# Optimization experiments

Measured on AMD Instinct MI355X. Metric: run time of the kernel, lower is better.

## Reference

```python
import jax, jax.numpy as jnp
import numpy as np

D_MODEL = 512
D_K = 64
D_V = 64
N_HEADS = 8
N = 4096
EPS = 1e-5


def setup_inputs() -> dict:
    key = jax.random.key(0)
    ks = jax.random.split(key, 12)
    s = 1.0 / np.sqrt(D_MODEL)
    return {
        "Q": jax.random.normal(ks[0], (N, D_MODEL), dtype=jnp.float32),
        "K": jax.random.normal(ks[1], (N, D_MODEL), dtype=jnp.float32),
        "V": jax.random.normal(ks[2], (N, D_MODEL), dtype=jnp.float32),
        "W_Q": jax.random.normal(ks[3], (D_K * N_HEADS, D_MODEL), dtype=jnp.float32) * s,
        "b_Q": jnp.zeros((D_K * N_HEADS,), jnp.float32),
        "W_K": jax.random.normal(ks[4], (D_K * N_HEADS, D_MODEL), dtype=jnp.float32) * s,
        "b_K": jnp.zeros((D_K * N_HEADS,), jnp.float32),
        "W_V": jax.random.normal(ks[5], (D_V * N_HEADS, D_MODEL), dtype=jnp.float32) * s,
        "b_V": jnp.zeros((D_V * N_HEADS,), jnp.float32),
        "W_O": jax.random.normal(ks[6], (D_MODEL, N_HEADS * D_V), dtype=jnp.float32) * s,
        "b_O": jnp.zeros((D_MODEL,), jnp.float32),
        "gamma": jnp.ones((D_MODEL,), jnp.float32),
        "beta": jnp.zeros((D_MODEL,), jnp.float32),
    }


def reference(Q, K, V, W_Q, b_Q, W_K, b_K, W_V, b_V, W_O, b_O, gamma, beta):
    n = Q.shape[0]
    # projections (torch Linear: x @ W.T + b), then split heads: [N, H, dk]
    Qs = (Q @ W_Q.T + b_Q).reshape(n, N_HEADS, D_K)
    Ks = (K @ W_K.T + b_K).reshape(n, N_HEADS, D_K)
    Vs = (V @ W_V.T + b_V).reshape(n, N_HEADS, D_V)
    # per-head scaled dot-product attention over the N dim, batched via einsum
    scores = jnp.einsum("nhd,mhd->hnm", Qs, Ks) / np.sqrt(D_K)  # [H, N, N]
    attn = jax.nn.softmax(scores, axis=-1)
    ctx = jnp.einsum("hnm,mhd->nhd", attn, Vs)  # [N, H, dv]
    context = ctx.reshape(n, N_HEADS * D_V)  # concat heads (matches torch.cat order)
    out = context @ W_O.T + b_O + Q  # output proj + residual
    # LayerNorm over last dim
    mu = jnp.mean(out, axis=-1, keepdims=True)
    var = jnp.mean((out - mu) ** 2, axis=-1, keepdims=True)
    return (out - mu) * jax.lax.rsqrt(var + EPS) * gamma + beta
```

## Files before the change

kernel.cpp:

```cpp
#include <hip/hip_runtime.h>
#include <cstdint>

#define N_TOK 4096
#define DMODEL 512
#define NHEADS 8
#define HDIM 64

typedef unsigned short u16;
typedef __bf16 bf16x8 __attribute__((ext_vector_type(8)));
typedef float f32x4 __attribute__((ext_vector_type(4)));

union U128 { uint4 u; bf16x8 b; u16 s[8]; };

__device__ __forceinline__ u16 f2bf(float f) {
  uint32_t u = __builtin_bit_cast(uint32_t, f);
  u += 0x7FFFu + ((u >> 16) & 1u);
  return (u16)(u >> 16);
}
__device__ __forceinline__ float bf2f(u16 s) {
  uint32_t u = ((uint32_t)s) << 16;
  return __builtin_bit_cast(float, u);
}

#if __has_builtin(__builtin_amdgcn_exp2f)
#define EXP2(x) __builtin_amdgcn_exp2f(x)
#else
#define EXP2(x) __expf((x) * 0.6931471805599453f)
#endif

__device__ __forceinline__ uint32_t cvtpk(float lo, float hi) {
  uint32_t r;
  asm("v_cvt_pk_bf16_f32 %0, %1, %2" : "=v"(r) : "v"(lo), "v"(hi));
  return r;
}

__device__ __forceinline__ void ldg2lds16(const void* g, void* s) {
  __builtin_amdgcn_global_load_lds(
      (const __attribute__((address_space(1))) void*)g,
      (__attribute__((address_space(3))) void*)s, 16, 0, 0);
}

__global__ __launch_bounds__(256) void cvt7_kernel(
    const float* __restrict__ Q, const float* __restrict__ K, const float* __restrict__ V,
    const float* __restrict__ WQ, const float* __restrict__ WK, const float* __restrict__ WV,
    const float* __restrict__ WO,
    u16* __restrict__ Qb, u16* __restrict__ Kb, u16* __restrict__ Vb,
    u16* __restrict__ WQb, u16* __restrict__ WKb, u16* __restrict__ WVb,
    u16* __restrict__ WOb)
{
  int b = blockIdx.x;
  const float* src; u16* dst; int rel;
  if      (b < 2048) { src = Q;  dst = Qb;  rel = b; }
  else if (b < 4096) { src = K;  dst = Kb;  rel = b - 2048; }
  else if (b < 6144) { src = V;  dst = Vb;  rel = b - 4096; }
  else if (b < 6400) { src = WQ; dst = WQb; rel = b - 6144; }
  else if (b < 6656) { src = WK; dst = WKb; rel = b - 6400; }
  else if (b < 6912) { src = WV; dst = WVb; rel = b - 6656; }
  else               { src = WO; dst = WOb; rel = b - 6912; }
  int i = (rel * 256 + threadIdx.x) * 4;
  float4 f = *(const float4*)(src + i);
  ushort4 o;
  o.x = f2bf(f.x); o.y = f2bf(f.y); o.z = f2bf(f.z); o.w = f2bf(f.w);
  *(ushort4*)(dst + i) = o;
}

__global__ __launch_bounds__(256) void proj3_kernel(
    const u16* __restrict__ Qb, const u16* __restrict__ Kb, const u16* __restrict__ Vb,
    const u16* __restrict__ WQb, const u16* __restrict__ WKb, const u16* __restrict__ WVb,
    const float* __restrict__ bQ, const float* __restrict__ bK, const float* __restrict__ bV,
    u16* __restrict__ Qs, u16* __restrict__ Ks, u16* __restrict__ Vt)
{
  const int z = blockIdx.z;
  const u16* A      = (z == 0) ? Qb : (z == 1) ? Kb : Vb;
  const u16* W      = (z == 0) ? WQb : (z == 1) ? WKb : WVb;
  const float* bias = (z == 0) ? bQ : (z == 1) ? bK : bV;

  const int m0 = blockIdx.x * 128;
  const int j0 = blockIdx.y * 64;
  const int tid = threadIdx.x;
  const int w = tid >> 6, lane = tid & 63, quad = lane >> 4, l = lane & 15;

  __shared__ bf16x8 sA[2][8][128];
  __shared__ bf16x8 sB[2][8][64];

  const f32x4 zero = {0.f, 0.f, 0.f, 0.f};
  f32x4 acc[2][4];
#pragma unroll
  for (int m = 0; m < 2; ++m)
#pragma unroll
    for (int s = 0; s < 4; ++s) acc[m][s] = zero;

  auto stage = [&](int kt, int buf) {
    const int k0 = kt * 64;
#pragma unroll
    for (int i = 0; i < 4; ++i) {
      const int chunk = 2 * w + (i >> 1), half = (i & 1) * 64;
      const u16* ag = A + (size_t)(m0 + half + lane) * DMODEL + k0 + chunk * 8;
      ldg2lds16(ag, (char*)&sA[buf][chunk][half]);
    }
#pragma unroll
    for (int i = 0; i < 2; ++i) {
      const int chunk = 2 * w + i;
      const u16* bg = W + (size_t)(j0 + lane) * DMODEL + k0 + chunk * 8;
      ldg2lds16(bg, (char*)&sB[buf][chunk][0]);
    }
  };

  stage(0, 0);
  __syncthreads();
  for (int kt = 0; kt < 8; ++kt) {
    const int buf = kt & 1;
    if (kt + 1 < 8) stage(kt + 1, buf ^ 1);
#pragma unroll
    for (int c = 0; c < 2; ++c) {
      bf16x8 af0 = sA[buf][c * 4 + quad][w * 32 + l];
      bf16x8 af1 = sA[buf][c * 4 + quad][w * 32 + 16 + l];
#pragma unroll
      for (int s = 0; s < 4; ++s) {
        bf16x8 bfb = sB[buf][c * 4 + quad][s * 16 + l];
        acc[0][s] = __builtin_amdgcn_mfma_f32_16x16x32_bf16(af0, bfb, acc[0][s], 0, 0, 0);
        acc[1][s] = __builtin_amdgcn_mfma_f32_16x16x32_bf16(af1, bfb, acc[1][s], 0, 0, 0);
      }
    }
    __syncthreads();
  }

#pragma unroll
  for (int m = 0; m < 2; ++m)
#pragma unroll
    for (int s = 0; s < 4; ++s) {
      int j = j0 + s * 16 + l;
      float bv = bias[j];
      int n0 = m0 + w * 32 + m * 16 + quad * 4;
      if (z < 2) {
        u16* Y = (z == 0) ? Qs : Ks;
#pragma unroll
        for (int r = 0; r < 4; ++r)
          Y[(size_t)(n0 + r) * DMODEL + j] = f2bf(acc[m][s][r] + bv);
      } else {
        ushort4 pk;
        pk.x = f2bf(acc[m][s][0] + bv); pk.y = f2bf(acc[m][s][1] + bv);
        pk.z = f2bf(acc[m][s][2] + bv); pk.w = f2bf(acc[m][s][3] + bv);
        *(ushort4*)(Vt + (size_t)j * N_TOK + n0) = pk;
      }
    }
}

__global__ __launch_bounds__(512, 4) void attn_kernel(
    const u16* __restrict__ Qs, const u16* __restrict__ Ks,
    const u16* __restrict__ Vt, u16* __restrict__ Opart, float* __restrict__ Lpart)
{
  const int hs = blockIdx.x;
  const int h = hs & 7, split = hs >> 3;
  const int qt = blockIdx.y;
  const int tid = threadIdx.x;
  const int w = tid >> 6, lane = tid & 63, quad = lane >> 4, l = lane & 15;

  __shared__ bf16x8 kch[2][8][64];
  __shared__ bf16x8 vch[2][8][64];
  __shared__ __align__(128) u16 pbuf[8][32][64];

  const int wq0 = qt * 256 + w * 32;

  bf16x8 qf[2][2];
#pragma unroll
  for (int c = 0; c < 2; ++c)
#pragma unroll
    for (int m = 0; m < 2; ++m) {
      U128 u;
      u.u = *(const uint4*)(Qs + (size_t)(wq0 + m * 16 + l) * DMODEL + h * HDIM + c * 32 + quad * 8);
#pragma unroll
      for (int j = 0; j < 8; ++j) u.s[j] = f2bf(bf2f(u.s[j]) * 0.18033688f);
      qf[c][m] = u.b;
    }

  U128 onesu;
#pragma unroll
  for (int j = 0; j < 8; ++j) onesu.s[j] = 0x3F80;

  const f32x4 zero = {0.f, 0.f, 0.f, 0.f};
  f32x4 o[2][4];
  f32x4 ol[2];
  ol[0] = zero; ol[1] = zero;
#pragma unroll
  for (int m = 0; m < 2; ++m)
#pragma unroll
    for (int s = 0; s < 4; ++s) o[m][s] = zero;

  auto stage = [&](int it, int buf) {
    const int j0 = split * 1024 + it * 64;
    if (w < 4) {
      const u16* kg = Ks + (size_t)(j0 + lane) * DMODEL + h * HDIM + w * 16;
      ldg2lds16(kg,     (char*)&kch[buf][2 * w][0]);
      ldg2lds16(kg + 8, (char*)&kch[buf][2 * w + 1][0]);
    } else {
      const int w2 = w - 4;
      const u16* vg = Vt + (size_t)(h * HDIM + lane) * N_TOK + j0 + w2 * 16;
      ldg2lds16(vg,     (char*)&vch[buf][2 * w2][0]);
      ldg2lds16(vg + 8, (char*)&vch[buf][2 * w2 + 1][0]);
    }
  };

  stage(0, 0);
  __syncthreads();

  const unsigned swz = (unsigned)((l & 7) << 4);

  for (int it = 0; it < 16; ++it) {
    const int buf = it & 1;
    if (it + 1 < 16) stage(it + 1, buf ^ 1);

#pragma unroll
    for (int kh = 0; kh < 2; ++kh) {
#pragma unroll
      for (int tt = 0; tt < 2; ++tt) {
        const int t = kh * 2 + tt;
        f32x4 sacc[2];
        sacc[0] = zero; sacc[1] = zero;
#pragma unroll
        for (int c = 0; c < 2; ++c) {
          bf16x8 kf = kch[buf][c * 4 + quad][t * 16 + l];
          sacc[0] = __builtin_amdgcn_mfma_f32_16x16x32_bf16(kf, qf[c][0], sacc[0], 0, 0, 0);
          sacc[1] = __builtin_amdgcn_mfma_f32_16x16x32_bf16(kf, qf[c][1], sacc[1], 0, 0, 0);
        }
#pragma unroll
        for (int m = 0; m < 2; ++m) {
          uint2 st;
          st.x = cvtpk(EXP2(sacc[m][0]), EXP2(sacc[m][1]));
          st.y = cvtpk(EXP2(sacc[m][2]), EXP2(sacc[m][3]));
          char* pb = (char*)&pbuf[w][m * 16 + l][0];
          *(uint2*)(pb + (((unsigned)(tt * 32 + quad * 8)) ^ swz)) = st;
        }
      }
      U128 pf0, pf1;
      const unsigned ro = ((unsigned)(quad * 16)) ^ swz;
      pf0.u = *(const uint4*)((const char*)&pbuf[w][l][0] + ro);
      pf1.u = *(const uint4*)((const char*)&pbuf[w][16 + l][0] + ro);
#pragma unroll
      for (int s = 0; s < 4; ++s) {
        bf16x8 vf = vch[buf][kh * 4 + quad][s * 16 + l];
        o[0][s] = __builtin_amdgcn_mfma_f32_16x16x32_bf16(pf0.b, vf, o[0][s], 0, 0, 0);
        o[1][s] = __builtin_amdgcn_mfma_f32_16x16x32_bf16(pf1.b, vf, o[1][s], 0, 0, 0);
      }
      ol[0] = __builtin_amdgcn_mfma_f32_16x16x32_bf16(pf0.b, onesu.b, ol[0], 0, 0, 0);
      ol[1] = __builtin_amdgcn_mfma_f32_16x16x32_bf16(pf1.b, onesu.b, ol[1], 0, 0, 0);
    }
    __syncthreads();
  }

  if (l == 0) {
    float* Lp = Lpart + ((size_t)split * NHEADS + h) * N_TOK + wq0;
#pragma unroll
    for (int m = 0; m < 2; ++m)
#pragma unroll
      for (int r = 0; r < 4; ++r)
        Lp[m * 16 + quad * 4 + r] = ol[m][r];
  }
  u16* Ob = Opart + ((size_t)(split * NHEADS + h) * N_TOK + wq0) * 64;
#pragma unroll
  for (int m = 0; m < 2; ++m)
#pragma unroll
    for (int s = 0; s < 4; ++s)
#pragma unroll
      for (int r = 0; r < 4; ++r)
        Ob[(size_t)(m * 16 + quad * 4 + r) * 64 + s * 16 + l] = f2bf(o[m][s][r]);
}

__global__ __launch_bounds__(256) void combine_kernel(
    const u16* __restrict__ Opart, const float* __restrict__ Lpart,
    u16* __restrict__ ctx)
{
  int idx = blockIdx.x * 256 + threadIdx.x;
  int n = idx >> 6;
  int c8 = idx & 63;
  int h = c8 >> 3;
  int vd0 = (c8 & 7) * 8;

  float acc[8] = {0, 0, 0, 0, 0, 0, 0, 0};
  float lsum = 0.f;
#pragma unroll
  for (int s = 0; s < 4; ++s) {
    U128 u;
    u.u = *(const uint4*)(Opart + ((size_t)(s * NHEADS + h) * N_TOK + n) * 64 + vd0);
#pragma unroll
    for (int j = 0; j < 8; ++j) acc[j] += bf2f(u.s[j]);
    lsum += Lpart[((size_t)s * NHEADS + h) * N_TOK + n];
  }
  float inv = 1.f / lsum;
  U128 u;
#pragma unroll
  for (int j = 0; j < 8; ++j) u.s[j] = f2bf(acc[j] * inv);
  *(uint4*)(ctx + (size_t)n * DMODEL + h * HDIM + vd0) = u.u;
}

__global__ __launch_bounds__(256) void gemmo_kernel(
    const u16* __restrict__ ctx, const u16* __restrict__ WOb,
    const float* __restrict__ bO, const float* __restrict__ resid,
    float* __restrict__ Y)
{
  const int m0 = blockIdx.x * 64;
  const int j0 = blockIdx.y * 64;
  const int tid = threadIdx.x;
  const int w = tid >> 6, lane = tid & 63, quad = lane >> 4, l = lane & 15;

  __shared__ bf16x8 sA[2][8][64];
  __shared__ bf16x8 sB[2][8][64];

  const f32x4 zero = {0.f, 0.f, 0.f, 0.f};
  f32x4 acc[4];
#pragma unroll
  for (int s = 0; s < 4; ++s) acc[s] = zero;

  auto stage = [&](int kt, int buf) {
    const int k0 = kt * 64;
#pragma unroll
    for (int i = 0; i < 2; ++i) {
      const int chunk = 2 * w + i;
      const u16* ag = ctx + (size_t)(m0 + lane) * DMODEL + k0 + chunk * 8;
      ldg2lds16(ag, (char*)&sA[buf][chunk][0]);
      const u16* bg = WOb + (size_t)(j0 + lane) * DMODEL + k0 + chunk * 8;
      ldg2lds16(bg, (char*)&sB[buf][chunk][0]);
    }
  };

  stage(0, 0);
  __syncthreads();
  for (int kt = 0; kt < 8; ++kt) {
    const int buf = kt & 1;
    if (kt + 1 < 8) stage(kt + 1, buf ^ 1);
#pragma unroll
    for (int c = 0; c < 2; ++c) {
      bf16x8 af = sA[buf][c * 4 + quad][w * 16 + l];
#pragma unroll
      for (int s = 0; s < 4; ++s) {
        bf16x8 bfb = sB[buf][c * 4 + quad][s * 16 + l];
        acc[s] = __builtin_amdgcn_mfma_f32_16x16x32_bf16(af, bfb, acc[s], 0, 0, 0);
      }
    }
    __syncthreads();
  }
#pragma unroll
  for (int s = 0; s < 4; ++s) {
    int j = j0 + s * 16 + l;
    float bv = bO[j];
    int n0 = m0 + w * 16 + quad * 4;
#pragma unroll
    for (int r = 0; r < 4; ++r)
      Y[(size_t)(n0 + r) * DMODEL + j] = acc[s][r] + bv + resid[(size_t)(n0 + r) * DMODEL + j];
  }
}

__global__ __launch_bounds__(256) void ln_kernel(
    const float* __restrict__ X, const float* __restrict__ gamma,
    const float* __restrict__ beta, float* __restrict__ Y)
{
  const int w = threadIdx.x >> 6, lane = threadIdx.x & 63;
  const int row = blockIdx.x * 4 + w;
  const float* x = X + (size_t)row * DMODEL + lane * 8;
  float4 a = *(const float4*)x;
  float4 b = *(const float4*)(x + 4);

  float s = a.x + a.y + a.z + a.w + b.x + b.y + b.z + b.w;
#pragma unroll
  for (int m = 1; m < 64; m <<= 1) s += __shfl_xor(s, m);
  float mu = s * (1.f / DMODEL);

  float d0 = a.x - mu, d1 = a.y - mu, d2 = a.z - mu, d3 = a.w - mu;
  float d4 = b.x - mu, d5 = b.y - mu, d6 = b.z - mu, d7 = b.w - mu;
  float v = d0*d0 + d1*d1 + d2*d2 + d3*d3 + d4*d4 + d5*d5 + d6*d6 + d7*d7;
#pragma unroll
  for (int m = 1; m < 64; m <<= 1) v += __shfl_xor(v, m);
  float sc = rsqrtf(v * (1.f / DMODEL) + 1e-5f);

  const float* g = gamma + lane * 8;
  const float* be = beta + lane * 8;
  float4 go = *(const float4*)g;
  float4 g1 = *(const float4*)(g + 4);
  float4 bo = *(const float4*)be;
  float4 b1 = *(const float4*)(be + 4);

  float4 y0, y1;
  y0.x = d0 * sc * go.x + bo.x;  y0.y = d1 * sc * go.y + bo.y;
  y0.z = d2 * sc * go.z + bo.z;  y0.w = d3 * sc * go.w + bo.w;
  y1.x = d4 * sc * g1.x + b1.x;  y1.y = d5 * sc * g1.y + b1.y;
  y1.z = d6 * sc * g1.z + b1.z;  y1.w = d7 * sc * g1.w + b1.w;

  float* yp = Y + (size_t)row * DMODEL + lane * 8;
  *(float4*)yp = y0;
  *(float4*)(yp + 4) = y1;
}

extern "C" void kernel_launch(void* const* d_in, const int* in_sizes, int n_in,
                              void* d_out, int out_size, void* d_ws, size_t ws_size,
                              hipStream_t stream)
{
  const float* Q     = (const float*)d_in[0];
  const float* K     = (const float*)d_in[1];
  const float* V     = (const float*)d_in[2];
  const float* WQ    = (const float*)d_in[3];
  const float* bQ    = (const float*)d_in[4];
  const float* WK    = (const float*)d_in[5];
  const float* bK    = (const float*)d_in[6];
  const float* WV    = (const float*)d_in[7];
  const float* bV    = (const float*)d_in[8];
  const float* WO    = (const float*)d_in[9];
  const float* bO    = (const float*)d_in[10];
  const float* gamma = (const float*)d_in[11];
  const float* beta  = (const float*)d_in[12];

  const size_t MB = 1ull << 20;
  char* ws = (char*)d_ws;
  u16* Qb   = (u16*)(ws + 0 * MB);
  u16* Kb   = (u16*)(ws + 4 * MB);
  u16* Vb   = (u16*)(ws + 8 * MB);
  u16* WQb  = (u16*)(ws + 12 * MB);
  u16* WKb  = (u16*)(ws + 12 * MB + 512 * 1024);
  u16* WVb  = (u16*)(ws + 13 * MB);
  u16* WOb  = (u16*)(ws + 13 * MB + 512 * 1024);
  u16* Qs   = (u16*)(ws + 14 * MB);
  u16* Ks   = (u16*)(ws + 18 * MB);
  u16* Vt   = (u16*)(ws + 22 * MB);
  u16* ctx  = (u16*)(ws + 26 * MB);
  u16* Opart = (u16*)(ws + 30 * MB);
  float* tmp = (float*)(ws + 30 * MB);
  float* Lpart = (float*)(ws + 46 * MB);
  float* out = (float*)d_out;

  cvt7_kernel<<<7168, 256, 0, stream>>>(Q, K, V, WQ, WK, WV, WO,
                                        Qb, Kb, Vb, WQb, WKb, WVb, WOb);
  proj3_kernel<<<dim3(32, 8, 3), 256, 0, stream>>>(Qb, Kb, Vb, WQb, WKb, WVb,
                                                   bQ, bK, bV, Qs, Ks, Vt);
  attn_kernel<<<dim3(32, 16), 512, 0, stream>>>(Qs, Ks, Vt, Opart, Lpart);
  combine_kernel<<<1024, 256, 0, stream>>>(Opart, Lpart, ctx);
  gemmo_kernel<<<dim3(64, 8), 256, 0, stream>>>(ctx, WOb, bO, Q, tmp);
  ln_kernel<<<1024, 256, 0, stream>>>(tmp, gamma, beta, out);
}
```

Before: 178.6 us.

## Fuse partial combine, output projection and LayerNorm into one kernel

Replaces the combine, output GEMM and LayerNorm kernels with a single kernel. Each 1024-thread block owns 16 token rows. It merges the split-attention partials straight into shared memory and streams all of W_O through double-buffered, XOR-swizzled LDS. It then applies bias, residual and LayerNorm with a block-wide reduction. This removes two launches and the global round trips for ctx and the fp32 pre-norm tensor. In exchange, every block rereads the full W_O, large LDS use limits occupancy to one block per CU, and variance is computed as E[x²]−μ², which is slightly less numerically robust.

```diff
diff --git a/kernel.cpp b/kernel.cpp
--- a/kernel.cpp
+++ b/kernel.cpp
@@ -266,128 +266,123 @@
         Ob[(size_t)(m * 16 + quad * 4 + r) * 64 + s * 16 + l] = f2bf(o[m][s][r]);
 }
 
-__global__ __launch_bounds__(256) void combine_kernel(
+__global__ __launch_bounds__(1024) void outfuse_kernel(
     const u16* __restrict__ Opart, const float* __restrict__ Lpart,
-    u16* __restrict__ ctx)
+    const u16* __restrict__ WOb, const float* __restrict__ bO,
+    const float* __restrict__ resid, const float* __restrict__ gamma,
+    const float* __restrict__ beta, float* __restrict__ Y)
 {
-  int idx = blockIdx.x * 256 + threadIdx.x;
-  int n = idx >> 6;
-  int c8 = idx & 63;
-  int h = c8 >> 3;
-  int vd0 = (c8 & 7) * 8;
-
-  float acc[8] = {0, 0, 0, 0, 0, 0, 0, 0};
-  float lsum = 0.f;
-#pragma unroll
-  for (int s = 0; s < 4; ++s) {
-    U128 u;
-    u.u = *(const uint4*)(Opart + ((size_t)(s * NHEADS + h) * N_TOK + n) * 64 + vd0);
-#pragma unroll
-    for (int j = 0; j < 8; ++j) acc[j] += bf2f(u.s[j]);
-    lsum += Lpart[((size_t)s * NHEADS + h) * N_TOK + n];
-  }
-  float inv = 1.f / lsum;
-  U128 u;
-#pragma unroll
-  for (int j = 0; j < 8; ++j) u.s[j] = f2bf(acc[j] * inv);
-  *(uint4*)(ctx + (size_t)n * DMODEL + h * HDIM + vd0) = u.u;
-}
-
-__global__ __launch_bounds__(256) void gemmo_kernel(
-    const u16* __restrict__ ctx, const u16* __restrict__ WOb,
-    const float* __restrict__ bO, const float* __restrict__ resid,
-    float* __restrict__ Y)
-{
-  const int m0 = blockIdx.x * 64;
-  const int j0 = blockIdx.y * 64;
+  __shared__ __align__(128) char smem[16384 + 2 * 65536];
+  bf16x8* sA = (bf16x8*)smem;
+  bf16x8* sB = (bf16x8*)(smem + 16384);
+  float* pls = (float*)smem;
+  float* plq = (float*)smem + 256;
+  float* mrow = (float*)smem + 512;
+
   const int tid = threadIdx.x;
   const int w = tid >> 6, lane = tid & 63, quad = lane >> 4, l = lane & 15;
-
-  __shared__ bf16x8 sA[2][8][64];
-  __shared__ bf16x8 sB[2][8][64];
+  const int n0 = blockIdx.x * 16;
+
+  auto stageB = [&](int kt, int buf) {
+#pragma unroll
+    for (int t = 0; t < 4; ++t) {
+      const int jb = w * 32 + t * 8;
+      const u16* g = WOb + (size_t)(jb + (lane >> 3)) * DMODEL + kt * 64
+                   + (((lane & 7) ^ (lane >> 3)) * 8);
+      ldg2lds16(g, (char*)&sB[(size_t)buf * 4096 + jb * 8]);
+    }
+  };
+
+  stageB(0, 0);
+
+  {
+    const int h = tid >> 7;
+    const int n = (tid >> 3) & 15;
+    const int vd0 = (tid & 7) * 8;
+    float a8[8] = {0, 0, 0, 0, 0, 0, 0, 0};
+    float lsum = 0.f;
+#pragma unroll
+    for (int s = 0; s < 4; ++s) {
+      U128 u;
+      u.u = *(const uint4*)(Opart + ((size_t)(s * NHEADS + h) * N_TOK + n0 + n) * 64 + vd0);
+#pragma unroll
+      for (int j = 0; j < 8; ++j) a8[j] += bf2f(u.s[j]);
+      lsum += Lpart[((size_t)s * NHEADS + h) * N_TOK + n0 + n];
+    }
+    float inv = 1.f / lsum;
+    U128 o;
+#pragma unroll
+    for (int j = 0; j < 8; ++j) o.s[j] = f2bf(a8[j] * inv);
+    const int col8 = h * 8 + (tid & 7);
+    *(uint4*)&sA[col8 * 16 + n] = o.u;
+  }
+  __syncthreads();
 
   const f32x4 zero = {0.f, 0.f, 0.f, 0.f};
-  f32x4 acc[4];
-#pragma unroll
-  for (int s = 0; s < 4; ++s) acc[s] = zero;
-
-  auto stage = [&](int kt, int buf) {
-    const int k0 = kt * 64;
-#pragma unroll
-    for (int i = 0; i < 2; ++i) {
-      const int chunk = 2 * w + i;
-      const u16* ag = ctx + (size_t)(m0 + lane) * DMODEL + k0 + chunk * 8;
-      ldg2lds16(ag, (char*)&sA[buf][chunk][0]);
-      const u16* bg = WOb + (size_t)(j0 + lane) * DMODEL + k0 + chunk * 8;
-      ldg2lds16(bg, (char*)&sB[buf][chunk][0]);
-    }
-  };
-
-  stage(0, 0);
-  __syncthreads();
+  f32x4 acc[2];
+  acc[0] = zero; acc[1] = zero;
+
   for (int kt = 0; kt < 8; ++kt) {
     const int buf = kt & 1;
-    if (kt + 1 < 8) stage(kt + 1, buf ^ 1);
+    if (kt + 1 < 8) stageB(kt + 1, buf ^ 1);
 #pragma unroll
     for (int c = 0; c < 2; ++c) {
-      bf16x8 af = sA[buf][c * 4 + quad][w * 16 + l];
-#pragma unroll
-      for (int s = 0; s < 4; ++s) {
-        bf16x8 bfb = sB[buf][c * 4 + quad][s * 16 + l];
+      bf16x8 af = sA[(kt * 8 + c * 4 + quad) * 16 + l];
+#pragma unroll
+      for (int s = 0; s < 2; ++s) {
+        const int j = w * 32 + s * 16 + l;
+        bf16x8 bfb = sB[(size_t)buf * 4096 + j * 8 + ((c * 4 + quad) ^ (l & 7))];
         acc[s] = __builtin_amdgcn_mfma_f32_16x16x32_bf16(af, bfb, acc[s], 0, 0, 0);
       }
     }
     __syncthreads();
   }
-#pragma unroll
-  for (int s = 0; s < 4; ++s) {
-    int j = j0 + s * 16 + l;
-    float bv = bO[j];
-    int n0 = m0 + w * 16 + quad * 4;
+
+  float vb[2][4];
+#pragma unroll
+  for (int s = 0; s < 2; ++s) {
+    const int j = w * 32 + s * 16 + l;
+    const float bv = bO[j];
 #pragma unroll
     for (int r = 0; r < 4; ++r)
-      Y[(size_t)(n0 + r) * DMODEL + j] = acc[s][r] + bv + resid[(size_t)(n0 + r) * DMODEL + j];
-  }
-}
-
-__global__ __launch_bounds__(256) void ln_kernel(
-    const float* __restrict__ X, const float* __restrict__ gamma,
-    const float* __restrict__ beta, float* __restrict__ Y)
-{
-  const int w = threadIdx.x >> 6, lane = threadIdx.x & 63;
-  const int row = blockIdx.x * 4 + w;
-  const float* x = X + (size_t)row * DMODEL + lane * 8;
-  float4 a = *(const float4*)x;
-  float4 b = *(const float4*)(x + 4);
-
-  float s = a.x + a.y + a.z + a.w + b.x + b.y + b.z + b.w;
-#pragma unroll
-  for (int m = 1; m < 64; m <<= 1) s += __shfl_xor(s, m);
-  float mu = s * (1.f / DMODEL);
-
-  float d0 = a.x - mu, d1 = a.y - mu, d2 = a.z - mu, d3 = a.w - mu;
-  float d4 = b.x - mu, d5 = b.y - mu, d6 = b.z - mu, d7 = b.w - mu;
-  float v = d0*d0 + d1*d1 + d2*d2 + d3*d3 + d4*d4 + d5*d5 + d6*d6 + d7*d7;
-#pragma unroll
-  for (int m = 1; m < 64; m <<= 1) v += __shfl_xor(v, m);
-  float sc = rsqrtf(v * (1.f / DMODEL) + 1e-5f);
-
-  const float* g = gamma + lane * 8;
-  const float* be = beta + lane * 8;
-  float4 go = *(const float4*)g;
-  float4 g1 = *(const float4*)(g + 4);
-  float4 bo = *(const float4*)be;
-  float4 b1 = *(const float4*)(be + 4);
-
-  float4 y0, y1;
-  y0.x = d0 * sc * go.x + bo.x;  y0.y = d1 * sc * go.y + bo.y;
-  y0.z = d2 * sc * go.z + bo.z;  y0.w = d3 * sc * go.w + bo.w;
-  y1.x = d4 * sc * g1.x + b1.x;  y1.y = d5 * sc * g1.y + b1.y;
-  y1.z = d6 * sc * g1.z + b1.z;  y1.w = d7 * sc * g1.w + b1.w;
-
-  float* yp = Y + (size_t)row * DMODEL + lane * 8;
-  *(float4*)yp = y0;
-  *(float4*)(yp + 4) = y1;
+      vb[s][r] = acc[s][r] + bv + resid[(size_t)(n0 + quad * 4 + r) * DMODEL + j];
+  }
+#pragma unroll
+  for (int r = 0; r < 4; ++r) {
+    float sm = vb[0][r] + vb[1][r];
+    float sq = vb[0][r] * vb[0][r] + vb[1][r] * vb[1][r];
+#pragma unroll
+    for (int mk = 1; mk < 16; mk <<= 1) {
+      sm += __shfl_xor(sm, mk);
+      sq += __shfl_xor(sq, mk);
+    }
+    if (l == 0) {
+      pls[(quad * 4 + r) * 16 + w] = sm;
+      plq[(quad * 4 + r) * 16 + w] = sq;
+    }
+  }
+  __syncthreads();
+  if (tid < 16) {
+    float sm = 0.f, sq = 0.f;
+#pragma unroll
+    for (int w2 = 0; w2 < 16; ++w2) { sm += pls[tid * 16 + w2]; sq += plq[tid * 16 + w2]; }
+    const float mu = sm * (1.f / DMODEL);
+    const float var = sq * (1.f / DMODEL) - mu * mu;
+    mrow[tid * 2]     = mu;
+    mrow[tid * 2 + 1] = rsqrtf(var + 1e-5f);
+  }
+  __syncthreads();
+#pragma unroll
+  for (int s = 0; s < 2; ++s) {
+    const int j = w * 32 + s * 16 + l;
+    const float gj = gamma[j], bj = beta[j];
+#pragma unroll
+    for (int r = 0; r < 4; ++r) {
+      const int row = quad * 4 + r;
+      const float mu = mrow[row * 2], sc = mrow[row * 2 + 1];
+      Y[(size_t)(n0 + row) * DMODEL + j] = (vb[s][r] - mu) * sc * gj + bj;
+    }
+  }
 }
 
 extern "C" void kernel_launch(void* const* d_in, const int* in_sizes, int n_in,
@@ -420,9 +415,7 @@
   u16* Qs   = (u16*)(ws + 14 * MB);
   u16* Ks   = (u16*)(ws + 18 * MB);
   u16* Vt   = (u16*)(ws + 22 * MB);
-  u16* ctx  = (u16*)(ws + 26 * MB);
   u16* Opart = (u16*)(ws + 30 * MB);
-  float* tmp = (float*)(ws + 30 * MB);
   float* Lpart = (float*)(ws + 46 * MB);
   float* out = (float*)d_out;
 
@@ -431,7 +424,6 @@
   proj3_kernel<<<dim3(32, 8, 3), 256, 0, stream>>>(Qb, Kb, Vb, WQb, WKb, WVb,
                                                    bQ, bK, bV, Qs, Ks, Vt);
   attn_kernel<<<dim3(32, 16), 512, 0, stream>>>(Qs, Ks, Vt, Opart, Lpart);
-  combine_kernel<<<1024, 256, 0, stream>>>(Opart, Lpart, ctx);
-  gemmo_kernel<<<dim3(64, 8), 256, 0, stream>>>(ctx, WOb, bO, Q, tmp);
-  ln_kernel<<<1024, 256, 0, stream>>>(tmp, gamma, beta, out);
-}
+  outfuse_kernel<<<256, 1024, 0, stream>>>(Opart, Lpart, WOb, bO, Q,
+                                           gamma, beta, out);
+}
```

Result: faster. 172.7 us (-3.3%).
